# Kernel optimization log

Hardware: AMD Instinct MI355X
Metric: run time of the kernel (lower is better)

The kernel has to match this reference:

```python
import jax, jax.numpy as jnp
import numpy as np

NUM_EXPERTS = 8
TOP_K = 2


def setup_inputs() -> dict:
    key = jax.random.key(0)
    k1, k2, k3, k4, k5 = jax.random.split(key, 5)
    H, F, E = 1024, 4096, NUM_EXPERTS
    s = 0.02
    return {
        "hidden_states": jax.random.normal(k1, (2, 2048, H), jnp.float32),
        "w_router": jax.random.normal(k2, (E, H), jnp.float32) * s,
        "w1": jax.random.normal(k3, (E, F, H), jnp.float32) * s,
        "w2": jax.random.normal(k4, (E, H, F), jnp.float32) * s,
        "w3": jax.random.normal(k5, (E, F, H), jnp.float32) * s,
    }


def reference(hidden_states, w_router, w1, w2, w3):
    B, S, H = hidden_states.shape
    x = hidden_states.reshape(-1, H)  # [T, H]
    T = x.shape[0]
    # router (nn.Linear, no bias): logits = x @ W^T
    router_logits = x @ w_router.T  # [T, E]
    probs = jax.nn.softmax(router_logits.astype(jnp.float32), axis=-1)
    top_w, top_e = jax.lax.top_k(probs, TOP_K)  # [T, K]
    top_w = top_w / jnp.sum(top_w, axis=-1, keepdims=True)
    top_w = top_w.astype(x.dtype)
    # dense per-token gate matrix [T, E]; zero where expert not selected
    gates = jnp.zeros((T, NUM_EXPERTS), x.dtype).at[
        jnp.arange(T)[:, None], top_e
    ].add(top_w)
    out = jnp.zeros_like(x)
    for e in range(NUM_EXPERTS):  # fixed small expert loop
        h = jax.nn.silu(x @ w1[e].T) * (x @ w3[e].T)  # [T, F]
        out = out + gates[:, e:e + 1] * (h @ w2[e].T)
    return out.reshape(B, S, H), router_logits
```

## Files before the change

### kernel.cpp

```cpp
#include <hip/hip_runtime.h>
#include <hip/hip_bf16.h>
#include <stdint.h>

#define T_TOK 4096
#define H_DIM 1024
#define F_DIM 4096
#define NE 8

typedef float    f32x4  __attribute__((ext_vector_type(4)));
typedef __bf16   bf16x8 __attribute__((ext_vector_type(8)));
typedef uint16_t u16x8  __attribute__((ext_vector_type(8)));

#define AS1 __attribute__((address_space(1)))
#define AS3 __attribute__((address_space(3)))

__device__ __forceinline__ uint16_t f2bf(float f) {
  return __builtin_bit_cast(uint16_t, __float2bfloat16(f));
}

__device__ __forceinline__ void gld16(const void* g, void* l) {
  __builtin_amdgcn_global_load_lds((const AS1 void*)g, (AS3 void*)l, 16, 0, 0);
}

__global__ __launch_bounds__(256) void router_k(
    const float* __restrict__ x, const float* __restrict__ wr,
    float* __restrict__ logits, uint16_t* __restrict__ xb,
    int* __restrict__ pairTok, float* __restrict__ pairGate,
    int* __restrict__ cnt)
{
  const int lane = threadIdx.x & 63;
  const int wid  = threadIdx.x >> 6;
  const int t    = blockIdx.x * 4 + wid;

  const float* xp = x + (size_t)t * H_DIM + lane * 16;
  f32x4 xv[4];
#pragma unroll
  for (int i = 0; i < 4; ++i) xv[i] = *(const f32x4*)(xp + 4 * i);

  u16x8 o0, o1;
#pragma unroll
  for (int j = 0; j < 4; ++j) {
    o0[j] = f2bf(xv[0][j]); o0[j + 4] = f2bf(xv[1][j]);
    o1[j] = f2bf(xv[2][j]); o1[j + 4] = f2bf(xv[3][j]);
  }
  uint16_t* xbp = xb + (size_t)t * H_DIM + lane * 16;
  *(u16x8*)xbp       = o0;
  *(u16x8*)(xbp + 8) = o1;

  float s[NE];
#pragma unroll
  for (int e = 0; e < NE; ++e) {
    const float* wp = wr + e * H_DIM + lane * 16;
    float acc = 0.f;
#pragma unroll
    for (int i = 0; i < 4; ++i) {
      f32x4 wv = *(const f32x4*)(wp + 4 * i);
#pragma unroll
      for (int j = 0; j < 4; ++j) acc += xv[i][j] * wv[j];
    }
#pragma unroll
    for (int off = 32; off > 0; off >>= 1) acc += __shfl_xor(acc, off, 64);
    s[e] = acc;
  }

  if (lane == 0) {
#pragma unroll
    for (int e = 0; e < NE; ++e) logits[t * NE + e] = s[e];
    int e1 = 0;
#pragma unroll
    for (int e = 1; e < NE; ++e) if (s[e] > s[e1]) e1 = e;
    int e2 = (e1 == 0) ? 1 : 0;
#pragma unroll
    for (int e = 0; e < NE; ++e)
      if (e != e1 && e != e2 && s[e] > s[e2]) e2 = e;
    const float d  = s[e2] - s[e1];
    const float g1 = 1.f / (1.f + __expf(d));
    const float g2 = 1.f - g1;
    int i1 = atomicAdd(cnt + e1, 1);
    pairTok[e1 * T_TOK + i1] = t;  pairGate[e1 * T_TOK + i1] = g1;
    int i2 = atomicAdd(cnt + e2, 1);
    pairTok[e2 * T_TOK + i2] = t;  pairGate[e2 * T_TOK + i2] = g2;
  }
}

__global__ void prefix_k(const int* __restrict__ cnt, int* __restrict__ base) {
  if (threadIdx.x == 0) {
    int b = 0;
#pragma unroll
    for (int e = 0; e < NE; ++e) { base[e] = b; b += cnt[e]; }
  }
}

__global__ __launch_bounds__(256, 2) void ffn1_k(
    const uint16_t* __restrict__ xb, const float* __restrict__ w1,
    const float* __restrict__ w3, uint16_t* __restrict__ hbuf,
    const int* __restrict__ pairTok, const int* __restrict__ cnt,
    const int* __restrict__ base)
{
  const int e    = blockIdx.z;
  const int cnte = cnt[e];
  const int m0   = blockIdx.y * 256;
  if (m0 >= cnte) return;
  const int n0   = blockIdx.x * 64;
  const int tid  = threadIdx.x;
  const int lane = tid & 63;
  const int wid  = tid >> 6;
  const int wm   = (wid >> 1) * 128;
  const int wn   = (wid & 1) * 32;

  __shared__ __align__(16) uint16_t lsA [256 * 64];
  __shared__ __align__(16) uint16_t lsB1[ 64 * 64];
  __shared__ __align__(16) uint16_t lsB3[ 64 * 64];

  const float* w1e = w1 + (size_t)e * F_DIM * H_DIM;
  const float* w3e = w3 + (size_t)e * F_DIM * H_DIM;

  const uint16_t* asrc[8];
#pragma unroll
  for (int q = 0; q < 8; ++q) {
    const int c = q * 256 + tid;
    const int row = c >> 3, pos = c & 7;
    const int kc  = pos ^ (row & 7);
    int ar = m0 + row; if (ar >= cnte) ar = cnte - 1;
    const int tok = pairTok[e * T_TOK + ar];
    asrc[q] = xb + (size_t)tok * H_DIM + kc * 8;
  }
  const float* b1src[2];
  const float* b3src[2];
  int bdst[2];
#pragma unroll
  for (int q = 0; q < 2; ++q) {
    const int c = q * 256 + tid;
    const int row = c >> 3, pos = c & 7;
    const int kc  = pos ^ (row & 7);
    bdst[q] = c * 8;
    b1src[q] = w1e + (size_t)(n0 + row) * H_DIM + kc * 8;
    b3src[q] = w3e + (size_t)(n0 + row) * H_DIM + kc * 8;
  }

  const f32x4 fz = {0.f, 0.f, 0.f, 0.f};
  f32x4 acc1[8][2], acc3[8][2];
#pragma unroll
  for (int i = 0; i < 8; ++i)
#pragma unroll
    for (int j = 0; j < 2; ++j) { acc1[i][j] = fz; acc3[i][j] = fz; }

  for (int kt = 0; kt < H_DIM; kt += 64) {
    __syncthreads();
#pragma unroll
    for (int q = 0; q < 8; ++q)
      gld16(asrc[q] + kt, &lsA[(q * 256 + tid) * 8]);
#pragma unroll
    for (int q = 0; q < 2; ++q) {
      const float* s1 = b1src[q] + kt;
      const float* s3 = b3src[q] + kt;
      f32x4 a0 = *(const f32x4*)s1;
      f32x4 a1 = *(const f32x4*)(s1 + 4);
      f32x4 c0 = *(const f32x4*)s3;
      f32x4 c1 = *(const f32x4*)(s3 + 4);
      u16x8 ob1, ob3;
#pragma unroll
      for (int j = 0; j < 4; ++j) {
        ob1[j] = f2bf(a0[j]); ob1[j + 4] = f2bf(a1[j]);
        ob3[j] = f2bf(c0[j]); ob3[j + 4] = f2bf(c1[j]);
      }
      *(u16x8*)&lsB1[bdst[q]] = ob1;
      *(u16x8*)&lsB3[bdst[q]] = ob3;
    }
    __syncthreads();
#pragma unroll
    for (int ks = 0; ks < 2; ++ks) {
      const int kg = ks * 4 + (lane >> 4);
      bf16x8 af[8], b1f[2], b3f[2];
#pragma unroll
      for (int i = 0; i < 8; ++i) {
        const int ar = wm + i * 16 + (lane & 15);
        af[i] = *(const bf16x8*)&lsA[ar * 64 + ((kg ^ (ar & 7)) * 8)];
      }
#pragma unroll
      for (int j = 0; j < 2; ++j) {
        const int br = wn + j * 16 + (lane & 15);
        b1f[j] = *(const bf16x8*)&lsB1[br * 64 + ((kg ^ (br & 7)) * 8)];
        b3f[j] = *(const bf16x8*)&lsB3[br * 64 + ((kg ^ (br & 7)) * 8)];
      }
#pragma unroll
      for (int i = 0; i < 8; ++i)
#pragma unroll
        for (int j = 0; j < 2; ++j) {
          acc1[i][j] = __builtin_amdgcn_mfma_f32_16x16x32_bf16(af[i], b1f[j], acc1[i][j], 0, 0, 0);
          acc3[i][j] = __builtin_amdgcn_mfma_f32_16x16x32_bf16(af[i], b3f[j], acc3[i][j], 0, 0, 0);
        }
    }
  }

  const int be = base[e];
#pragma unroll
  for (int i = 0; i < 8; ++i) {
#pragma unroll
    for (int r = 0; r < 4; ++r) {
      const int lrow = m0 + wm + i * 16 + (lane >> 4) * 4 + r;
      if (lrow < cnte) {
        uint16_t* hp = hbuf + (size_t)(be + lrow) * F_DIM + n0 + wn + (lane & 15);
#pragma unroll
        for (int j = 0; j < 2; ++j) {
          const float a  = acc1[i][j][r];
          const float hv = (a / (1.f + __expf(-a))) * acc3[i][j][r];
          hp[j * 16] = f2bf(hv);
        }
      }
    }
  }
}

__global__ __launch_bounds__(256, 2) void ffn2_k(
    const uint16_t* __restrict__ hbuf, const float* __restrict__ w2,
    float* __restrict__ out, const int* __restrict__ pairTok,
    const float* __restrict__ pairGate, const int* __restrict__ cnt,
    const int* __restrict__ base)
{
  const int e    = blockIdx.z;
  const int cnte = cnt[e];
  const int m0   = blockIdx.y * 256;
  if (m0 >= cnte) return;
  const int n0   = blockIdx.x * 128;
  const int tid  = threadIdx.x;
  const int lane = tid & 63;
  const int wid  = tid >> 6;
  const int wm   = (wid >> 1) * 128;
  const int wn   = (wid & 1) * 64;

  __shared__ __align__(16) uint16_t lsA[256 * 64];
  __shared__ __align__(16) uint16_t lsB[128 * 64];

  const int be = base[e];
  const float* w2e = w2 + (size_t)e * H_DIM * F_DIM;

  const uint16_t* asrc[8];
#pragma unroll
  for (int q = 0; q < 8; ++q) {
    const int c = q * 256 + tid;
    const int row = c >> 3, pos = c & 7;
    const int kc  = pos ^ (row & 7);
    int rr = m0 + row; if (rr >= cnte) rr = cnte - 1;
    asrc[q] = hbuf + (size_t)(be + rr) * F_DIM + kc * 8;
  }
  const float* bsrc[4];
  int bdst[4];
#pragma unroll
  for (int q = 0; q < 4; ++q) {
    const int c = q * 256 + tid;
    const int row = c >> 3, pos = c & 7;
    const int kc  = pos ^ (row & 7);
    bdst[q] = c * 8;
    bsrc[q] = w2e + (size_t)(n0 + row) * F_DIM + kc * 8;
  }

  const f32x4 fz = {0.f, 0.f, 0.f, 0.f};
  f32x4 acc[8][4];
#pragma unroll
  for (int i = 0; i < 8; ++i)
#pragma unroll
    for (int j = 0; j < 4; ++j) acc[i][j] = fz;

  for (int kt = 0; kt < F_DIM; kt += 64) {
    __syncthreads();
#pragma unroll
    for (int q = 0; q < 8; ++q)
      gld16(asrc[q] + kt, &lsA[(q * 256 + tid) * 8]);
#pragma unroll
    for (int q = 0; q < 4; ++q) {
      const float* sb = bsrc[q] + kt;
      f32x4 b0 = *(const f32x4*)sb;
      f32x4 b1 = *(const f32x4*)(sb + 4);
      u16x8 ob;
#pragma unroll
      for (int j = 0; j < 4; ++j) { ob[j] = f2bf(b0[j]); ob[j + 4] = f2bf(b1[j]); }
      *(u16x8*)&lsB[bdst[q]] = ob;
    }
    __syncthreads();
#pragma unroll
    for (int ks = 0; ks < 2; ++ks) {
      const int kg = ks * 4 + (lane >> 4);
      bf16x8 af[8], bf[4];
#pragma unroll
      for (int i = 0; i < 8; ++i) {
        const int ar = wm + i * 16 + (lane & 15);
        af[i] = *(const bf16x8*)&lsA[ar * 64 + ((kg ^ (ar & 7)) * 8)];
      }
#pragma unroll
      for (int j = 0; j < 4; ++j) {
        const int br = wn + j * 16 + (lane & 15);
        bf[j] = *(const bf16x8*)&lsB[br * 64 + ((kg ^ (br & 7)) * 8)];
      }
#pragma unroll
      for (int i = 0; i < 8; ++i)
#pragma unroll
        for (int j = 0; j < 4; ++j)
          acc[i][j] = __builtin_amdgcn_mfma_f32_16x16x32_bf16(af[i], bf[j], acc[i][j], 0, 0, 0);
    }
  }

#pragma unroll
  for (int i = 0; i < 8; ++i) {
#pragma unroll
    for (int r = 0; r < 4; ++r) {
      const int lrow = m0 + wm + i * 16 + (lane >> 4) * 4 + r;
      if (lrow < cnte) {
        const int   t = pairTok [e * T_TOK + lrow];
        const float g = pairGate[e * T_TOK + lrow];
        float* op = out + (size_t)t * H_DIM + n0 + wn + (lane & 15);
#pragma unroll
        for (int j = 0; j < 4; ++j)
          unsafeAtomicAdd(op + j * 16, g * acc[i][j][r]);
      }
    }
  }
}

extern "C" void kernel_launch(void* const* d_in, const int* in_sizes, int n_in,
                              void* d_out, int out_size, void* d_ws, size_t ws_size,
                              hipStream_t stream)
{
  const float* x  = (const float*)d_in[0];
  const float* wr = (const float*)d_in[1];
  const float* w1 = (const float*)d_in[2];
  const float* w2 = (const float*)d_in[3];
  const float* w3 = (const float*)d_in[4];
  float* out    = (float*)d_out;
  float* logits = out + (size_t)T_TOK * H_DIM;

  uint8_t* ws = (uint8_t*)d_ws;
  const size_t XB_OFF   = 0;
  const size_t HB_OFF   = XB_OFF + (size_t)T_TOK * H_DIM * 2;
  const size_t PT_OFF   = HB_OFF + (size_t)2 * T_TOK * F_DIM * 2;
  const size_t PG_OFF   = PT_OFF + (size_t)NE * T_TOK * 4;
  const size_t CNT_OFF  = PG_OFF + (size_t)NE * T_TOK * 4;
  const size_t BASE_OFF = CNT_OFF + 64;
  const size_t NEED     = BASE_OFF + 64;
  if (ws_size < NEED) return;

  uint16_t* xb      = (uint16_t*)(ws + XB_OFF);
  uint16_t* hb      = (uint16_t*)(ws + HB_OFF);
  int*      pairTok = (int*)(ws + PT_OFF);
  float*    pairGate= (float*)(ws + PG_OFF);
  int*      cnt     = (int*)(ws + CNT_OFF);
  int*      basep   = (int*)(ws + BASE_OFF);

  hipMemsetAsync(out, 0, (size_t)T_TOK * H_DIM * sizeof(float), stream);
  hipMemsetAsync(cnt, 0, 64, stream);
  router_k<<<T_TOK / 4, 256, 0, stream>>>(x, wr, logits, xb, pairTok, pairGate, cnt);
  prefix_k<<<1, 64, 0, stream>>>(cnt, basep);
  ffn1_k<<<dim3(F_DIM / 64, T_TOK / 256, NE), 256, 0, stream>>>(xb, w1, w3, hb, pairTok, cnt, basep);
  ffn2_k<<<dim3(H_DIM / 128, T_TOK / 256, NE), 256, 0, stream>>>(hb, w2, out, pairTok, pairGate, cnt, basep);
}
```

Measured before the change: 481.9 us.

## Compact expert tiles into flat grid and replace atomic scatter with combine kernel

The M dimension is flattened across experts, with each expert's rows padded to 256, so the GEMM grids launch only MG_BLKS tiles instead of 16 per expert, most of which exited early before. The gate weight moves into the ffn1 epilogue, and ffn2 writes per-pair bf16 outputs to a buffer instead of doing float atomic adds into the output. A new combine kernel gathers each token's two expert rows and sums them, which also removes the output memset. In exchange it adds a launch and extra traffic, and it rounds the ffn2 result to bf16 before combining, which loses precision.

```diff
diff --git a/kernel.cpp b/kernel.cpp
--- a/kernel.cpp
+++ b/kernel.cpp
@@ -6,6 +6,7 @@
 #define H_DIM 1024
 #define F_DIM 4096
 #define NE 8
+#define MG_BLKS 40
 
 typedef float    f32x4  __attribute__((ext_vector_type(4)));
 typedef __bf16   bf16x8 __attribute__((ext_vector_type(8)));
@@ -26,7 +27,7 @@
     const float* __restrict__ x, const float* __restrict__ wr,
     float* __restrict__ logits, uint16_t* __restrict__ xb,
     int* __restrict__ pairTok, float* __restrict__ pairGate,
-    int* __restrict__ cnt)
+    int* __restrict__ tokSlot, int* __restrict__ cnt)
 {
   const int lane = threadIdx.x & 63;
   const int wid  = threadIdx.x >> 6;
@@ -80,6 +81,8 @@
     pairTok[e1 * T_TOK + i1] = t;  pairGate[e1 * T_TOK + i1] = g1;
     int i2 = atomicAdd(cnt + e2, 1);
     pairTok[e2 * T_TOK + i2] = t;  pairGate[e2 * T_TOK + i2] = g2;
+    int4 sl; sl.x = e1; sl.y = i1; sl.z = e2; sl.w = i2;
+    ((int4*)tokSlot)[t] = sl;
   }
 }
 
@@ -87,20 +90,24 @@
   if (threadIdx.x == 0) {
     int b = 0;
 #pragma unroll
-    for (int e = 0; e < NE; ++e) { base[e] = b; b += cnt[e]; }
+    for (int e = 0; e < NE; ++e) { base[e] = b; b += (cnt[e] + 255) & ~255; }
+    base[NE] = b;
   }
 }
 
 __global__ __launch_bounds__(256, 2) void ffn1_k(
     const uint16_t* __restrict__ xb, const float* __restrict__ w1,
     const float* __restrict__ w3, uint16_t* __restrict__ hbuf,
-    const int* __restrict__ pairTok, const int* __restrict__ cnt,
-    const int* __restrict__ base)
-{
-  const int e    = blockIdx.z;
+    const int* __restrict__ pairTok, const float* __restrict__ pairGate,
+    const int* __restrict__ cnt, const int* __restrict__ base)
+{
+  const int mg0 = blockIdx.y * 256;
+  if (mg0 >= base[NE]) return;
+  int e = 0;
+#pragma unroll
+  for (int k = 1; k < NE; ++k) if (mg0 >= base[k]) e = k;
+  const int m0   = mg0 - base[e];
   const int cnte = cnt[e];
-  const int m0   = blockIdx.y * 256;
-  if (m0 >= cnte) return;
   const int n0   = blockIdx.x * 64;
   const int tid  = threadIdx.x;
   const int lane = tid & 63;
@@ -111,6 +118,12 @@
   __shared__ __align__(16) uint16_t lsA [256 * 64];
   __shared__ __align__(16) uint16_t lsB1[ 64 * 64];
   __shared__ __align__(16) uint16_t lsB3[ 64 * 64];
+  __shared__ float lsG[256];
+
+  {
+    const int rr = m0 + tid;
+    lsG[tid] = (rr < cnte) ? pairGate[e * T_TOK + rr] : 0.f;
+  }
 
   const float* w1e = w1 + (size_t)e * F_DIM * H_DIM;
   const float* w3e = w3 + (size_t)e * F_DIM * H_DIM;
@@ -200,11 +213,12 @@
     for (int r = 0; r < 4; ++r) {
       const int lrow = m0 + wm + i * 16 + (lane >> 4) * 4 + r;
       if (lrow < cnte) {
+        const float g = lsG[lrow - m0];
         uint16_t* hp = hbuf + (size_t)(be + lrow) * F_DIM + n0 + wn + (lane & 15);
 #pragma unroll
         for (int j = 0; j < 2; ++j) {
           const float a  = acc1[i][j][r];
-          const float hv = (a / (1.f + __expf(-a))) * acc3[i][j][r];
+          const float hv = g * (a / (1.f + __expf(-a))) * acc3[i][j][r];
           hp[j * 16] = f2bf(hv);
         }
       }
@@ -214,14 +228,16 @@
 
 __global__ __launch_bounds__(256, 2) void ffn2_k(
     const uint16_t* __restrict__ hbuf, const float* __restrict__ w2,
-    float* __restrict__ out, const int* __restrict__ pairTok,
-    const float* __restrict__ pairGate, const int* __restrict__ cnt,
+    uint16_t* __restrict__ y, const int* __restrict__ cnt,
     const int* __restrict__ base)
 {
-  const int e    = blockIdx.z;
+  const int mg0 = blockIdx.y * 256;
+  if (mg0 >= base[NE]) return;
+  int e = 0;
+#pragma unroll
+  for (int k = 1; k < NE; ++k) if (mg0 >= base[k]) e = k;
+  const int m0   = mg0 - base[e];
   const int cnte = cnt[e];
-  const int m0   = blockIdx.y * 256;
-  if (m0 >= cnte) return;
   const int n0   = blockIdx.x * 128;
   const int tid  = threadIdx.x;
   const int lane = tid & 63;
@@ -306,15 +322,37 @@
     for (int r = 0; r < 4; ++r) {
       const int lrow = m0 + wm + i * 16 + (lane >> 4) * 4 + r;
       if (lrow < cnte) {
-        const int   t = pairTok [e * T_TOK + lrow];
-        const float g = pairGate[e * T_TOK + lrow];
-        float* op = out + (size_t)t * H_DIM + n0 + wn + (lane & 15);
+        uint16_t* yp = y + (size_t)(be + lrow) * H_DIM + n0 + wn + (lane & 15);
 #pragma unroll
         for (int j = 0; j < 4; ++j)
-          unsafeAtomicAdd(op + j * 16, g * acc[i][j][r]);
-      }
-    }
-  }
+          yp[j * 16] = f2bf(acc[i][j][r]);
+      }
+    }
+  }
+}
+
+__global__ __launch_bounds__(256) void combine_k(
+    const uint16_t* __restrict__ y, const int* __restrict__ tokSlot,
+    const int* __restrict__ base, float* __restrict__ out)
+{
+  const int t = blockIdx.x * 2 + (threadIdx.x >> 7);
+  const int c = (threadIdx.x & 127) * 8;
+  const int4 s = ((const int4*)tokSlot)[t];
+  const uint16_t* y1 = y + (size_t)(base[s.x] + s.y) * H_DIM + c;
+  const uint16_t* y2 = y + (size_t)(base[s.z] + s.w) * H_DIM + c;
+  const u16x8 a = *(const u16x8*)y1;
+  const u16x8 b = *(const u16x8*)y2;
+  float* op = out + (size_t)t * H_DIM + c;
+  f32x4 o0, o1;
+#pragma unroll
+  for (int j = 0; j < 4; ++j) {
+    o0[j] = __bfloat162float(__hip_bfloat16_raw{a[j]}) +
+            __bfloat162float(__hip_bfloat16_raw{b[j]});
+    o1[j] = __bfloat162float(__hip_bfloat16_raw{a[j + 4]}) +
+            __bfloat162float(__hip_bfloat16_raw{b[j + 4]});
+  }
+  *(f32x4*)op       = o0;
+  *(f32x4*)(op + 4) = o1;
 }
 
 extern "C" void kernel_launch(void* const* d_in, const int* in_sizes, int n_in,
@@ -330,26 +368,31 @@
   float* logits = out + (size_t)T_TOK * H_DIM;
 
   uint8_t* ws = (uint8_t*)d_ws;
+  const size_t PADROWS  = (size_t)MG_BLKS * 256;
   const size_t XB_OFF   = 0;
   const size_t HB_OFF   = XB_OFF + (size_t)T_TOK * H_DIM * 2;
-  const size_t PT_OFF   = HB_OFF + (size_t)2 * T_TOK * F_DIM * 2;
+  const size_t Y_OFF    = HB_OFF + PADROWS * F_DIM * 2;
+  const size_t PT_OFF   = Y_OFF + PADROWS * H_DIM * 2;
   const size_t PG_OFF   = PT_OFF + (size_t)NE * T_TOK * 4;
-  const size_t CNT_OFF  = PG_OFF + (size_t)NE * T_TOK * 4;
+  const size_t TS_OFF   = PG_OFF + (size_t)NE * T_TOK * 4;
+  const size_t CNT_OFF  = TS_OFF + (size_t)T_TOK * 16;
   const size_t BASE_OFF = CNT_OFF + 64;
   const size_t NEED     = BASE_OFF + 64;
   if (ws_size < NEED) return;
 
   uint16_t* xb      = (uint16_t*)(ws + XB_OFF);
   uint16_t* hb      = (uint16_t*)(ws + HB_OFF);
+  uint16_t* yb      = (uint16_t*)(ws + Y_OFF);
   int*      pairTok = (int*)(ws + PT_OFF);
   float*    pairGate= (float*)(ws + PG_OFF);
+  int*      tokSlot = (int*)(ws + TS_OFF);
   int*      cnt     = (int*)(ws + CNT_OFF);
   int*      basep   = (int*)(ws + BASE_OFF);
 
-  hipMemsetAsync(out, 0, (size_t)T_TOK * H_DIM * sizeof(float), stream);
   hipMemsetAsync(cnt, 0, 64, stream);
-  router_k<<<T_TOK / 4, 256, 0, stream>>>(x, wr, logits, xb, pairTok, pairGate, cnt);
+  router_k<<<T_TOK / 4, 256, 0, stream>>>(x, wr, logits, xb, pairTok, pairGate, tokSlot, cnt);
   prefix_k<<<1, 64, 0, stream>>>(cnt, basep);
-  ffn1_k<<<dim3(F_DIM / 64, T_TOK / 256, NE), 256, 0, stream>>>(xb, w1, w3, hb, pairTok, cnt, basep);
-  ffn2_k<<<dim3(H_DIM / 128, T_TOK / 256, NE), 256, 0, stream>>>(hb, w2, out, pairTok, pairGate, cnt, basep);
-}
+  ffn1_k<<<dim3(F_DIM / 64, MG_BLKS, 1), 256, 0, stream>>>(xb, w1, w3, hb, pairTok, pairGate, cnt, basep);
+  ffn2_k<<<dim3(H_DIM / 128, MG_BLKS, 1), 256, 0, stream>>>(hb, w2, yb, cnt, basep);
+  combine_k<<<T_TOK / 2, 256, 0, stream>>>(yb, tokSlot, basep, out);
+}
```

After: 470.2 us. -2.4%, faster.
